# Performance work log

Measured on AMD Instinct MI355X. Metric: run time of the kernel, lower is better.

Reference implementation:

```python
import jax, jax.numpy as jnp
import numpy as np

PLOGIT_INIT = 1.5

def setup_inputs() -> dict:
    key = jax.random.key(0)
    B, C, H, W = 32, 256, 64, 64
    x = jax.random.normal(key, (B, C, H, W), dtype=jnp.float32)
    plogit = jnp.full((C,), PLOGIT_INIT, dtype=jnp.float32)  # learned param (post channel-expansion)
    return {"input": x, "plogit": plogit}


def reference(input, plogit):
    B, C = input.shape[0], input.shape[1]
    x = input.reshape(B * C, -1)                       # [B*C, HW]  (to_cw)
    s = jnp.sort(x, axis=-1)                           # per-row full sort
    N = s.shape[1]
    p = jax.nn.sigmoid(plogit)                         # [C]
    # torch: p.view(1,-1).repeat(B,1).view(-1) -> channel-major tiling over batch
    p_full = jnp.tile(p, B)                            # [B*C]
    # torch indexes with int(N * p.data[0] -/+ 0.02): a single scalar column index
    p0 = jax.lax.stop_gradient(p[0])
    i_low = jnp.clip((N * (p0 - 0.02)).astype(jnp.int32), 0, N - 1)
    i_high = jnp.clip((N * (p0 + 0.02)).astype(jnp.int32), 0, N - 1)
    x_low = jax.lax.stop_gradient(jnp.take(s, i_low, axis=1))    # [B*C], detached
    x_high = jax.lax.stop_gradient(jnp.take(s, i_high, axis=1))  # [B*C], detached
    thr = x_low + (x_high - x_low) * p_full            # linear interp, grad flows via p
    thr = thr.reshape(B, C, 1, 1)                      # from_cw
    return jax.nn.relu(input - thr)
```

## Files before the change

kernel.cpp:

```cpp
#include <hip/hip_runtime.h>
#include <math.h>

#define NTHREADS 256
#define NELEM    4096
#define EPL      32
#define NREPA    8
#define NREPB    2
#define HSTRIDE  260
#define ASIZE    (NREPA * HSTRIDE)
#define BSIZE    (NREPB * HSTRIDE)
#define ROWLDS   (ASIZE + BSIZE)

__device__ __forceinline__ unsigned f2ord(float f) {
    unsigned u = __float_as_uint(f);
    return (u & 0x80000000u) ? ~u : (u | 0x80000000u);
}
__device__ __forceinline__ float ord2f(unsigned k) {
    unsigned u = (k & 0x80000000u) ? (k ^ 0x80000000u) : ~k;
    return __uint_as_float(u);
}

struct Pick2 { unsigned a, b; };

template <int NR>
__device__ __forceinline__ Pick2 wave_pick2(const unsigned* region, int lane,
                                            unsigned rA, unsigned rB) {
    unsigned s0 = 0, s1 = 0, s2 = 0, s3 = 0;
    #pragma unroll
    for (int rep = 0; rep < NR; ++rep) {
        uint4 h = ((const uint4*)(region + rep * HSTRIDE))[lane];
        s0 += h.x; s1 += h.y; s2 += h.z; s3 += h.w;
    }
    unsigned lp1 = s0, lp2 = s0 + s1, lp3 = s0 + s1 + s2, tot = lp3 + s3;
    unsigned scan = tot;
    #pragma unroll
    for (int off = 1; off < 64; off <<= 1) {
        unsigned v = __shfl_up(scan, off, 64);
        if (lane >= off) scan += v;
    }
    unsigned ex = scan - tot;
    unsigned base[4] = {ex, ex + lp1, ex + lp2, ex + lp3};
    unsigned cnt[4]  = {s0, s1, s2, s3};
    unsigned resA = 0, resB = 0;
    bool fA = false, fB = false;
    #pragma unroll
    for (int j = 0; j < 4; ++j) {
        if (rA >= base[j] && rA < base[j] + cnt[j]) {
            resA = ((unsigned)(4 * lane + j) << 12) | (rA - base[j]); fA = true;
        }
        if (rB >= base[j] && rB < base[j] + cnt[j]) {
            resB = ((unsigned)(4 * lane + j) << 12) | (rB - base[j]); fB = true;
        }
    }
    unsigned long long mA = __ballot(fA);
    unsigned long long mB = __ballot(fB);
    Pick2 r;
    r.a = __shfl(resA, (int)(__ffsll((long long)mA) - 1), 64);
    r.b = __shfl(resB, (int)(__ffsll((long long)mB) - 1), 64);
    return r;
}

__global__ void __launch_bounds__(NTHREADS)
xsrelu_kernel(const float* __restrict__ x, const float* __restrict__ plogit,
              float* __restrict__ out, int C) {
    __shared__ __align__(16) unsigned hist[2][ROWLDS];

    const int wid   = threadIdx.x >> 6;
    const int lane  = threadIdx.x & 63;
    const int rhalf = wid & 1;
    const int rloc  = wid >> 1;
    const int row   = blockIdx.x * 2 + rloc;
    const int rlane = rhalf * 64 + lane;

    const float4* xr = (const float4*)(x + (size_t)row * NELEM);
    unsigned k[EPL];
    #pragma unroll
    for (int j = 0; j < EPL / 4; ++j) {
        float4 v = xr[j * 128 + rlane];
        k[4 * j + 0] = f2ord(v.x);
        k[4 * j + 1] = f2ord(v.y);
        k[4 * j + 2] = f2ord(v.z);
        k[4 * j + 3] = f2ord(v.w);
    }

    float p0 = 1.0f / (1.0f + expf(-plogit[0]));
    float pc = 1.0f / (1.0f + expf(-plogit[row % C]));
    int kLow  = min(max((int)((float)NELEM * (p0 - 0.02f)), 0), NELEM - 1);
    int kHigh = min(max((int)((float)NELEM * (p0 + 0.02f)), 0), NELEM - 1);

    unsigned* hA  = hist[rloc];
    unsigned* hB  = hA + ASIZE;
    unsigned* myA = hA + (rhalf * 4 + (lane & 3)) * HSTRIDE;
    unsigned* myB = hB + rhalf * HSTRIDE;

    unsigned prefA = 0u, prefB = 0u, known = 0u;
    unsigned rA = (unsigned)kLow, rB = (unsigned)kHigh;
    bool diverged = false;

    #pragma unroll 1
    for (int shift = 24; shift >= 0; shift -= 8) {
        uint4* hz = (uint4*)hA;
        #pragma unroll 1
        for (int i = rlane; i < ROWLDS / 4; i += 128)
            hz[i] = make_uint4(0u, 0u, 0u, 0u);
        __syncthreads();

        #pragma unroll
        for (int j = 0; j < EPL; ++j) {
            unsigned kk = k[j];
            if ((kk & known) == prefA)
                atomicAdd(&myA[(kk >> shift) & 0xFFu], 1u);
        }
        if (diverged) {
            #pragma unroll
            for (int j = 0; j < EPL; ++j) {
                unsigned kk = k[j];
                if ((kk & known) == prefB)
                    atomicAdd(&myB[(kk >> shift) & 0xFFu], 1u);
            }
        }
        __syncthreads();

        Pick2 p = wave_pick2<NREPA>(hA, lane, rA, diverged ? rA : rB);
        unsigned pA = p.a, pB = p.b;
        if (diverged)
            pB = wave_pick2<NREPB>(hB, lane, rB, rB).a;
        unsigned bA = pA >> 12, bB = pB >> 12;
        prefA |= bA << shift;  rA = pA & 0xFFFu;
        prefB |= bB << shift;  rB = pB & 0xFFFu;
        diverged = diverged || (bA != bB);
        known |= 0xFFu << shift;
        __syncthreads();
    }

    float xlow  = ord2f(prefA);
    float xhigh = ord2f(prefB);
    float thr = xlow + (xhigh - xlow) * pc;

    float4* outr = (float4*)(out + (size_t)row * NELEM);
    #pragma unroll
    for (int j = 0; j < EPL / 4; ++j) {
        float4 o;
        o.x = fmaxf(ord2f(k[4 * j + 0]) - thr, 0.0f);
        o.y = fmaxf(ord2f(k[4 * j + 1]) - thr, 0.0f);
        o.z = fmaxf(ord2f(k[4 * j + 2]) - thr, 0.0f);
        o.w = fmaxf(ord2f(k[4 * j + 3]) - thr, 0.0f);
        outr[j * 128 + rlane] = o;
    }
}

extern "C" void kernel_launch(void* const* d_in, const int* in_sizes, int n_in,
                              void* d_out, int out_size, void* d_ws, size_t ws_size,
                              hipStream_t stream) {
    const float* x      = (const float*)d_in[0];
    const float* plogit = (const float*)d_in[1];
    float* out          = (float*)d_out;
    int C    = in_sizes[1];
    int rows = in_sizes[0] / NELEM;
    xsrelu_kernel<<<rows / 2, NTHREADS, 0, stream>>>(x, plogit, out, C);
}
```

Measured before the change: 239.0 us.

## Use one row per block with lighter histogram passes and DPP scan

Measured after the change: 234.3 us. -2.0%, faster.

```diff
diff --git a/kernel.cpp b/kernel.cpp
--- a/kernel.cpp
+++ b/kernel.cpp
@@ -1,15 +1,14 @@
 #include <hip/hip_runtime.h>
 #include <math.h>
 
-#define NTHREADS 256
+#define NTHREADS 128
 #define NELEM    4096
 #define EPL      32
-#define NREPA    8
-#define NREPB    2
+#define NREP1    8
 #define HSTRIDE  260
-#define ASIZE    (NREPA * HSTRIDE)
-#define BSIZE    (NREPB * HSTRIDE)
-#define ROWLDS   (ASIZE + BSIZE)
+#define AREG     (NREP1 * HSTRIDE)
+#define BREG     (2 * HSTRIDE)
+#define LDSW     (AREG + BREG)
 
 __device__ __forceinline__ unsigned f2ord(float f) {
     unsigned u = __float_as_uint(f);
@@ -18,6 +17,16 @@
 __device__ __forceinline__ float ord2f(unsigned k) {
     unsigned u = (k & 0x80000000u) ? (k ^ 0x80000000u) : ~k;
     return __uint_as_float(u);
+}
+
+__device__ __forceinline__ unsigned iscan_dpp(unsigned v) {
+    v += (unsigned)__builtin_amdgcn_update_dpp(0, (int)v, 0x111, 0xF, 0xF, false);
+    v += (unsigned)__builtin_amdgcn_update_dpp(0, (int)v, 0x112, 0xF, 0xF, false);
+    v += (unsigned)__builtin_amdgcn_update_dpp(0, (int)v, 0x114, 0xF, 0xF, false);
+    v += (unsigned)__builtin_amdgcn_update_dpp(0, (int)v, 0x118, 0xF, 0xF, false);
+    v += (unsigned)__builtin_amdgcn_update_dpp(0, (int)v, 0x142, 0xA, 0xF, false);
+    v += (unsigned)__builtin_amdgcn_update_dpp(0, (int)v, 0x143, 0xC, 0xF, false);
+    return v;
 }
 
 struct Pick2 { unsigned a, b; };
@@ -31,15 +40,10 @@
         uint4 h = ((const uint4*)(region + rep * HSTRIDE))[lane];
         s0 += h.x; s1 += h.y; s2 += h.z; s3 += h.w;
     }
-    unsigned lp1 = s0, lp2 = s0 + s1, lp3 = s0 + s1 + s2, tot = lp3 + s3;
-    unsigned scan = tot;
-    #pragma unroll
-    for (int off = 1; off < 64; off <<= 1) {
-        unsigned v = __shfl_up(scan, off, 64);
-        if (lane >= off) scan += v;
-    }
-    unsigned ex = scan - tot;
-    unsigned base[4] = {ex, ex + lp1, ex + lp2, ex + lp3};
+    unsigned tot = s0 + s1 + s2 + s3;
+    unsigned inc = iscan_dpp(tot);
+    unsigned ex  = inc - tot;
+    unsigned base[4] = {ex, ex + s0, ex + s0 + s1, ex + s0 + s1 + s2};
     unsigned cnt[4]  = {s0, s1, s2, s3};
     unsigned resA = 0, resB = 0;
     bool fA = false, fB = false;
@@ -55,28 +59,26 @@
     unsigned long long mA = __ballot(fA);
     unsigned long long mB = __ballot(fB);
     Pick2 r;
-    r.a = __shfl(resA, (int)(__ffsll((long long)mA) - 1), 64);
-    r.b = __shfl(resB, (int)(__ffsll((long long)mB) - 1), 64);
+    r.a = (unsigned)__builtin_amdgcn_readlane((int)resA, (int)(__ffsll((long long)mA) - 1));
+    r.b = (unsigned)__builtin_amdgcn_readlane((int)resB, (int)(__ffsll((long long)mB) - 1));
     return r;
 }
 
 __global__ void __launch_bounds__(NTHREADS)
 xsrelu_kernel(const float* __restrict__ x, const float* __restrict__ plogit,
               float* __restrict__ out, int C) {
-    __shared__ __align__(16) unsigned hist[2][ROWLDS];
+    __shared__ __align__(16) unsigned hist[LDSW];
 
-    const int wid   = threadIdx.x >> 6;
-    const int lane  = threadIdx.x & 63;
-    const int rhalf = wid & 1;
-    const int rloc  = wid >> 1;
-    const int row   = blockIdx.x * 2 + rloc;
-    const int rlane = rhalf * 64 + lane;
+    const int tid  = threadIdx.x;
+    const int wid  = tid >> 6;
+    const int lane = tid & 63;
+    const int row  = blockIdx.x;
 
     const float4* xr = (const float4*)(x + (size_t)row * NELEM);
     unsigned k[EPL];
     #pragma unroll
     for (int j = 0; j < EPL / 4; ++j) {
-        float4 v = xr[j * 128 + rlane];
+        float4 v = xr[j * 128 + tid];
         k[4 * j + 0] = f2ord(v.x);
         k[4 * j + 1] = f2ord(v.y);
         k[4 * j + 2] = f2ord(v.z);
@@ -88,28 +90,47 @@
     int kLow  = min(max((int)((float)NELEM * (p0 - 0.02f)), 0), NELEM - 1);
     int kHigh = min(max((int)((float)NELEM * (p0 + 0.02f)), 0), NELEM - 1);
 
-    unsigned* hA  = hist[rloc];
-    unsigned* hB  = hA + ASIZE;
-    unsigned* myA = hA + (rhalf * 4 + (lane & 3)) * HSTRIDE;
-    unsigned* myB = hB + rhalf * HSTRIDE;
+    unsigned* hA  = hist;
+    unsigned* hB  = hist + AREG;
+    unsigned* my1 = hA + (wid * 4 + (lane & 3)) * HSTRIDE;
+    unsigned* myT = hA + wid * HSTRIDE;
+    unsigned* myB = hB + wid * HSTRIDE;
 
-    unsigned prefA = 0u, prefB = 0u, known = 0u;
-    unsigned rA = (unsigned)kLow, rB = (unsigned)kHigh;
-    bool diverged = false;
+    unsigned prefA = 0u, prefB = 0u, known = 0xFF000000u;
+    unsigned rA, rB;
+    bool diverged;
+
+    {
+        uint4* z = (uint4*)(hA + wid * 4 * HSTRIDE);
+        #pragma unroll 1
+        for (int i = lane; i < HSTRIDE; i += 64) z[i] = make_uint4(0u, 0u, 0u, 0u);
+        #pragma unroll
+        for (int j = 0; j < EPL; ++j)
+            atomicAdd(&my1[k[j] >> 24], 1u);
+        __syncthreads();
+        Pick2 p = wave_pick2<NREP1>(hA, lane, (unsigned)kLow, (unsigned)kHigh);
+        unsigned bA = p.a >> 12, bB = p.b >> 12;
+        prefA = bA << 24;  rA = p.a & 0xFFFu;
+        prefB = bB << 24;  rB = p.b & 0xFFFu;
+        diverged = (bA != bB);
+        __syncthreads();
+    }
 
     #pragma unroll 1
-    for (int shift = 24; shift >= 0; shift -= 8) {
-        uint4* hz = (uint4*)hA;
+    for (int shift = 16; shift >= 0; shift -= 8) {
+        uint4* z = (uint4*)myT;
         #pragma unroll 1
-        for (int i = rlane; i < ROWLDS / 4; i += 128)
-            hz[i] = make_uint4(0u, 0u, 0u, 0u);
-        __syncthreads();
-
+        for (int i = lane; i < HSTRIDE / 4; i += 64) z[i] = make_uint4(0u, 0u, 0u, 0u);
+        if (diverged) {
+            uint4* zb = (uint4*)myB;
+            #pragma unroll 1
+            for (int i = lane; i < HSTRIDE / 4; i += 64) zb[i] = make_uint4(0u, 0u, 0u, 0u);
+        }
         #pragma unroll
         for (int j = 0; j < EPL; ++j) {
             unsigned kk = k[j];
             if ((kk & known) == prefA)
-                atomicAdd(&myA[(kk >> shift) & 0xFFu], 1u);
+                atomicAdd(&myT[(kk >> shift) & 0xFFu], 1u);
         }
         if (diverged) {
             #pragma unroll
@@ -120,11 +141,10 @@
             }
         }
         __syncthreads();
-
-        Pick2 p = wave_pick2<NREPA>(hA, lane, rA, diverged ? rA : rB);
+        Pick2 p = wave_pick2<2>(hA, lane, rA, diverged ? rA : rB);
         unsigned pA = p.a, pB = p.b;
         if (diverged)
-            pB = wave_pick2<NREPB>(hB, lane, rB, rB).a;
+            pB = wave_pick2<2>(hB, lane, rB, rB).a;
         unsigned bA = pA >> 12, bB = pB >> 12;
         prefA |= bA << shift;  rA = pA & 0xFFFu;
         prefB |= bB << shift;  rB = pB & 0xFFFu;
@@ -145,7 +165,7 @@
         o.y = fmaxf(ord2f(k[4 * j + 1]) - thr, 0.0f);
         o.z = fmaxf(ord2f(k[4 * j + 2]) - thr, 0.0f);
         o.w = fmaxf(ord2f(k[4 * j + 3]) - thr, 0.0f);
-        outr[j * 128 + rlane] = o;
+        outr[j * 128 + tid] = o;
     }
 }
 
@@ -157,5 +177,5 @@
     float* out          = (float*)d_out;
     int C    = in_sizes[1];
     int rows = in_sizes[0] / NELEM;
-    xsrelu_kernel<<<rows / 2, NTHREADS, 0, stream>>>(x, plogit, out, C);
+    xsrelu_kernel<<<rows, NTHREADS, 0, stream>>>(x, plogit, out, C);
 }
```
